# Kernel optimization log

Measured on AMD Instinct MI355X. Metric: run time of the kernel, lower is better.

The kernel has to match this reference:

```python
import jax, jax.numpy as jnp
import numpy as np

EPS = 1e-5
GROUPS = 32


def conv2d(x, w, b):
    # x: [N,C,H,W], w: [O,I,3,3] (or 1x1), stride 1, padding 'same' for 3x3
    kh = w.shape[2]
    pad = (kh - 1) // 2
    y = jax.lax.conv_general_dilated(x, w, (1, 1), ((pad, pad), (pad, pad)),
                                     dimension_numbers=('NCHW', 'OIHW', 'NCHW'))
    return y + b[None, :, None, None]


def group_norm(x, g, b):
    N, C, H, W = x.shape
    xr = x.reshape(N, GROUPS, C // GROUPS, H, W)
    mu = xr.mean(axis=(2, 3, 4), keepdims=True)
    var = xr.var(axis=(2, 3, 4), keepdims=True)
    xr = (xr - mu) / jnp.sqrt(var + EPS)
    return xr.reshape(N, C, H, W) * g[None, :, None, None] + b[None, :, None, None]


def batch_norm(x, g, b):
    # training-mode BatchNorm2d: batch statistics over (N,H,W)
    mu = x.mean(axis=(0, 2, 3), keepdims=True)
    var = x.var(axis=(0, 2, 3), keepdims=True)
    return (x - mu) / jnp.sqrt(var + EPS) * g[None, :, None, None] + b[None, :, None, None]


def binary_activation(x):
    # STE: forward sign(x), backward through piecewise poly out3
    out_fwd = jnp.sign(x)
    m1 = (x < -1).astype(x.dtype)
    m2 = (x < 0).astype(x.dtype)
    m3 = (x < 1).astype(x.dtype)
    out1 = -1.0 * m1 + (x * x + 2.0 * x) * (1.0 - m1)
    out2 = out1 * m2 + (-x * x + 2.0 * x) * (1.0 - m2)
    out3 = out2 * m3 + 1.0 * (1.0 - m3)
    return jax.lax.stop_gradient(out_fwd - out3) + out3


def hard_binary_conv(x, w, b):
    # per-output-channel scaling * sign(w), STE through clipped weights
    scale = jax.lax.stop_gradient(jnp.mean(jnp.abs(w), axis=(1, 2, 3), keepdims=True))
    bw_ng = scale * jnp.sign(w)
    clipped = jnp.clip(w, -1.0, 1.0)
    bw = jax.lax.stop_gradient(bw_ng - clipped) + clipped
    return conv2d(x, bw, b)


def learnable_bias(x, emb, w, b):
    bias = jax.nn.silu(emb) @ w.T + b  # [B, C]
    return x + bias[:, :, None, None]


def _forward(c, x, emb,
             rb_gn1_g, rb_gn1_b, rb_conv1_w, rb_conv1_b, rb_emb_w, rb_emb_b,
             rb_gn2_g, rb_gn2_b, rb_conv2_w, rb_conv2_b,
             m1_w, m1_b, bconv_w, bconv_b, bn_g, bn_b,
             m2_w, m2_b, prelu_a, m3_w, m3_b):
    # ResBlock (skip = Identity since out_channels == channels)
    h = conv2d(jax.nn.silu(group_norm(c, rb_gn1_g, rb_gn1_b)), rb_conv1_w, rb_conv1_b)
    eo = jax.nn.silu(emb) @ rb_emb_w.T + rb_emb_b          # [B, 2*C]
    scale, shift = jnp.split(eo[:, :, None, None], 2, axis=1)
    h = group_norm(h, rb_gn2_g, rb_gn2_b) * (1.0 + scale) + shift
    h = conv2d(jax.nn.silu(h), rb_conv2_w, rb_conv2_b)
    c2 = c + h
    # concat + bias + STE binarize + binary conv + BN + channel-pool residual + PReLU
    xc = jnp.concatenate([x, c2], axis=1)                   # [B, 2C, H, W]
    out = learnable_bias(xc, emb, m1_w, m1_b)
    out = binary_activation(out)
    out = hard_binary_conv(out, bconv_w, bconv_b)
    out = batch_norm(out, bn_g, bn_b)
    N, C2, H, W = xc.shape
    out = out + xc.reshape(N, C2 // 2, 2, H, W).mean(axis=2)  # channel mean pooling
    out = learnable_bias(out, emb, m2_w, m2_b)
    out = jnp.where(out >= 0, out, prelu_a[None, :, None, None] * out)  # PReLU
    out = learnable_bias(out, emb, m3_w, m3_b)
    return out


def setup_inputs() -> dict:
    key = jax.random.key(0)
    ks = jax.random.split(key, 24)
    B, C, EMB, H, W = 8, 128, 512, 64, 64
    IN2 = 2 * C
    n = lambda k, s, sc=0.05: jax.random.normal(k, s, dtype=jnp.float32) * sc
    return {
        'c': jax.random.normal(ks[0], (B, C, H, W), dtype=jnp.float32),
        'x': jax.random.normal(ks[1], (B, C, H, W), dtype=jnp.float32),
        'emb': jax.random.normal(ks[2], (B, EMB), dtype=jnp.float32),
        'rb_gn1_g': jnp.ones((C,), jnp.float32), 'rb_gn1_b': jnp.zeros((C,), jnp.float32),
        'rb_conv1_w': n(ks[3], (C, C, 3, 3)), 'rb_conv1_b': n(ks[4], (C,)),
        'rb_emb_w': n(ks[5], (2 * C, EMB)), 'rb_emb_b': n(ks[6], (2 * C,)),
        'rb_gn2_g': jnp.ones((C,), jnp.float32), 'rb_gn2_b': jnp.zeros((C,), jnp.float32),
        'rb_conv2_w': n(ks[7], (C, C, 3, 3)), 'rb_conv2_b': n(ks[8], (C,)),
        'm1_w': n(ks[9], (IN2, EMB)), 'm1_b': n(ks[10], (IN2,)),
        'bconv_w': jax.random.uniform(ks[11], (C, IN2, 3, 3), dtype=jnp.float32) * 0.001,
        'bconv_b': n(ks[12], (C,)),
        'bn_g': jnp.ones((C,), jnp.float32), 'bn_b': jnp.zeros((C,), jnp.float32),
        'm2_w': n(ks[13], (C, EMB)), 'm2_b': n(ks[14], (C,)),
        'prelu_a': jnp.full((C,), 0.25, jnp.float32),
        'm3_w': n(ks[15], (C, EMB)), 'm3_b': n(ks[16], (C,)),
    }


def reference(c, x, emb,
              rb_gn1_g, rb_gn1_b, rb_conv1_w, rb_conv1_b, rb_emb_w, rb_emb_b,
              rb_gn2_g, rb_gn2_b, rb_conv2_w, rb_conv2_b,
              m1_w, m1_b, bconv_w, bconv_b, bn_g, bn_b,
              m2_w, m2_b, prelu_a, m3_w, m3_b):
    return _forward(c, x, emb,
                    rb_gn1_g, rb_gn1_b, rb_conv1_w, rb_conv1_b, rb_emb_w, rb_emb_b,
                    rb_gn2_g, rb_gn2_b, rb_conv2_w, rb_conv2_b,
                    m1_w, m1_b, bconv_w, bconv_b, bn_g, bn_b,
                    m2_w, m2_b, prelu_a, m3_w, m3_b)
```

## Files before the change

### kernel.cpp

```cpp
#include <hip/hip_runtime.h>
#include <stdint.h>


#define B_   8
#define C_   128
#define C2_  256
#define HW_  4096
#define EMB_ 512
#define EPS_ 1e-5f

typedef int   v16i __attribute__((ext_vector_type(16)));
typedef float v16f __attribute__((ext_vector_type(16)));
typedef short v8s  __attribute__((ext_vector_type(8)));
typedef int   v4i  __attribute__((ext_vector_type(4)));

#define COLB 272
#define LDSZ (3 * 66 * COLB)

__device__ __forceinline__ float silu(float v) {
    return v * __builtin_amdgcn_rcpf(1.f + __expf(-v));
}
__device__ __forceinline__ unsigned short f2bf(float f) {
    unsigned int x = __float_as_uint(f);
    return (unsigned short)((x + 0x7FFFu + ((x >> 16) & 1u)) >> 16);
}
__device__ __forceinline__ int8_t sgn8(float v) {
    return (v > 0.f) ? (int8_t)1 : ((v < 0.f) ? (int8_t)(-1) : (int8_t)0);
}

__global__ __launch_bounds__(256) void k_prep(
    const float* __restrict__ w, int8_t* __restrict__ sgn,
    float* __restrict__ alpha, float* __restrict__ bnS, float* __restrict__ bnQ,
    float* __restrict__ gnS, float* __restrict__ gnQ,
    const float* __restrict__ w1, const float* __restrict__ w2,
    unsigned short* __restrict__ Wc1, unsigned short* __restrict__ Wc2,
    const float* __restrict__ emb,
    const float* __restrict__ ew, const float* __restrict__ ebb,
    const float* __restrict__ m1w, const float* __restrict__ m1b,
    const float* __restrict__ m2w, const float* __restrict__ m2b,
    const float* __restrict__ m3w, const float* __restrict__ m3b,
    float* __restrict__ eo, float* __restrict__ b1,
    float* __restrict__ b2, float* __restrict__ b3,
    const float* __restrict__ gin, const float* __restrict__ g1w,
    const float* __restrict__ g1b, unsigned short* __restrict__ act1) {
    __shared__ float red[256];
    const int blk = blockIdx.x, tid = threadIdx.x;
    if (blk < 128) {
        const int o = blk;
        if (o == 0 && tid < 128) { bnS[tid] = 0.f; bnQ[tid] = 0.f; }
        if (o == 1) { gnS[tid] = 0.f; }
        if (o == 2) { gnQ[tid] = 0.f; }
        const float* wr = w + (size_t)o * (C2_ * 9);
        float s = 0.f;
        for (int i = tid; i < C2_ * 9; i += 256) s += fabsf(wr[i]);
        red[tid] = s;
        __syncthreads();
        for (int st = 128; st > 0; st >>= 1) {
            if (tid < st) red[tid] += red[tid + st];
            __syncthreads();
        }
        if (tid == 0) alpha[o] = red[0] / (float)(C2_ * 9);
        for (int kk = 0; kk < 9; ++kk) {
            float v = wr[tid * 9 + kk];
            sgn[((size_t)(kk * 16 + (tid >> 4)) * C_ + o) * 16 + (tid & 15)] = sgn8(v);
        }
    } else if (blk < 704) {
        int i = (blk - 128) * 256 + tid;
        int co = i / (C_ * 9);
        int rem = i - co * (C_ * 9);
        int ci = rem / 9, kk = rem - ci * 9;
        size_t d = ((size_t)(kk * 16 + (ci >> 3)) * C_ + co) * 8 + (ci & 7);
        Wc1[d] = f2bf(w1[i]);
        Wc2[d] = f2bf(w2[i]);
    } else if (blk < 896) {
        const int o = (blk - 704) * 4 + (tid >> 6);
        const int l = tid & 63;
        const float* wv;
        float bias;
        float* dst;
        int dstride;
        if (o < 256)      { wv = ew  + (size_t)o * EMB_;              bias = ebb[o];    dst = eo + o;  dstride = 256; }
        else if (o < 512) { int r = o - 256; wv = m1w + (size_t)r * EMB_; bias = m1b[r]; dst = b1 + r; dstride = 256; }
        else if (o < 640) { int r = o - 512; wv = m2w + (size_t)r * EMB_; bias = m2b[r]; dst = b2 + r; dstride = 128; }
        else              { int r = o - 640; wv = m3w + (size_t)r * EMB_; bias = m3b[r]; dst = b3 + r; dstride = 128; }
        const float4 wa = *(const float4*)(wv + 8 * l);
        const float4 wb = *(const float4*)(wv + 8 * l + 4);
#pragma unroll
        for (int b = 0; b < B_; ++b) {
            const float* s = emb + b * EMB_ + 8 * l;
            float4 sa = *(const float4*)(s);
            float4 sb = *(const float4*)(s + 4);
            float p = wa.x * silu(sa.x) + wa.y * silu(sa.y) + wa.z * silu(sa.z) + wa.w * silu(sa.w) +
                      wb.x * silu(sb.x) + wb.y * silu(sb.y) + wb.z * silu(sb.z) + wb.w * silu(sb.w);
#pragma unroll
            for (int off = 32; off > 0; off >>= 1) p += __shfl_down(p, off, 64);
            if (l == 0) dst[b * dstride] = bias + p;
        }
    } else {
        const int bb = blk - 896;
        const int n = bb >> 5, grp = bb & 31;
        const size_t base = ((size_t)(n * C_ + grp * 4)) << 12;
        float sum = 0.f, sq = 0.f;
        const float4* in4 = (const float4*)(gin + base);
        for (int i = tid; i < 4096; i += 256) {
            float4 v = in4[i];
            sum += v.x + v.y + v.z + v.w;
            sq += v.x * v.x + v.y * v.y + v.z * v.z + v.w * v.w;
        }
#pragma unroll
        for (int off = 32; off > 0; off >>= 1) {
            sum += __shfl_xor(sum, off, 64);
            sq  += __shfl_xor(sq, off, 64);
        }
        if ((tid & 63) == 0) { red[tid >> 6] = sum; red[8 + (tid >> 6)] = sq; }
        __syncthreads();
        sum = red[0] + red[1] + red[2] + red[3];
        sq  = red[8] + red[9] + red[10] + red[11];
        const float mu = sum * (1.f / 16384.f);
        const float rstd = rsqrtf(sq * (1.f / 16384.f) - mu * mu + EPS_);
        float gg[4], bb4[4];
#pragma unroll
        for (int j = 0; j < 4; ++j) { gg[j] = g1w[grp * 4 + j]; bb4[j] = g1b[grp * 4 + j]; }
        for (int hw = tid; hw < HW_; hw += 256) {
            union { unsigned short u[4]; uint2 v; } pk;
#pragma unroll
            for (int j = 0; j < 4; ++j) {
                float v = gin[base + ((size_t)j << 12) + hw];
                pk.u[j] = f2bf(silu((v - mu) * rstd * gg[j] + bb4[j]));
            }
            *(uint2*)(act1 + ((size_t)(n * HW_ + hw)) * C_ + grp * 4) = pk.v;
        }
    }
}

__device__ __forceinline__ void stage_rows(char* lds, const char* rs0,
                                           const char* rs1, const char* rs2) {
    const int tid = threadIdx.x;
    const char* rs[3] = {rs0, rs1, rs2};
    if (tid < 96) {
        int r = tid / 32, q = tid & 31;
        int c = (q >> 4) ? 65 : 0, o = q & 15;
        *(float4*)(lds + (r * 66 + c) * COLB + o * 16) = make_float4(0.f, 0.f, 0.f, 0.f);
    }
#pragma unroll
    for (int u = 0; u < 12; ++u) {
        int idx = u * 256 + tid;
        int r = idx >> 10, rem = idx & 1023;
        int x = rem >> 4, o = rem & 15;
        char* dst = lds + (r * 66 + x + 1) * COLB + o * 16;
        if (rs[r]) *(float4*)dst = *(const float4*)(rs[r] + x * 256 + o * 16);
        else       *(float4*)dst = make_float4(0.f, 0.f, 0.f, 0.f);
    }
}

__global__ __launch_bounds__(256) void k_conv1(const unsigned short* __restrict__ act,
                                               const unsigned short* __restrict__ Wc,
                                               const float* __restrict__ bias,
                                               float* __restrict__ out,
                                               float* __restrict__ gnS,
                                               float* __restrict__ gnQ) {
    __shared__ __align__(16) char lds[LDSZ];
    const int y = blockIdx.x;
    const int n = blockIdx.y;
    const char* base = (const char*)(act + ((size_t)n * 64) * 64 * C_);
    stage_rows(lds,
               (y > 0)  ? base + (size_t)(y - 1) * 16384 : nullptr,
               base + (size_t)y * 16384,
               (y < 63) ? base + (size_t)(y + 1) * 16384 : nullptr);
    __syncthreads();

    const int w = threadIdx.x >> 6;
    const int l = threadIdx.x & 63;
    const int lm = l & 31;
    const int lh = l >> 5;

    v16f acc0, acc1;
#pragma unroll
    for (int i = 0; i < 16; ++i) { acc0[i] = 0.f; acc1[i] = 0.f; }

#pragma unroll
    for (int kk = 0; kk < 9; ++kk) {
        const int r = kk / 3, dx = kk % 3 - 1;
        const char* col0 = lds + (r * 66 + lm + 1 + dx) * COLB + 16 * lh;
        const char* col1 = col0 + 32 * COLB;
        const unsigned short* wbase = Wc + (size_t)(kk * 16 + lh) * C_ * 8 + (32 * w + lm) * 8;
#pragma unroll
        for (int cb = 0; cb < 8; ++cb) {
            v8s a = *(const v8s*)(wbase + (size_t)(2 * cb) * C_ * 8);
            v8s b0 = *(const v8s*)(col0 + 32 * cb);
            v8s b1 = *(const v8s*)(col1 + 32 * cb);
            acc0 = __builtin_amdgcn_mfma_f32_32x32x16_bf16(a, b0, acc0, 0, 0, 0);
            acc1 = __builtin_amdgcn_mfma_f32_32x32x16_bf16(a, b1, acc1, 0, 0, 0);
        }
    }
    float pr[16], qr[16];
#pragma unroll
    for (int r = 0; r < 16; ++r) {
        const int row = (r & 3) + 8 * (r >> 2) + 4 * lh;
        const int co = 32 * w + row;
        const float bv = bias[co];
        const size_t o = (((size_t)n * C_ + co) << 12) + (y << 6);
        float v0 = acc0[r] + bv, v1 = acc1[r] + bv;
        out[o + lm] = v0;
        out[o + 32 + lm] = v1;
        pr[r] = v0 + v1;
        qr[r] = v0 * v0 + v1 * v1;
    }
    __syncthreads();
    float* ldsS = (float*)lds;
    float* ldsQ = (float*)lds + 128;
#pragma unroll
    for (int r = 0; r < 16; ++r) {
        float p = pr[r], q = qr[r];
#pragma unroll
        for (int m = 16; m > 0; m >>= 1) {
            p += __shfl_xor(p, m, 64);
            q += __shfl_xor(q, m, 64);
        }
        if (lm == 0) {
            const int row = (r & 3) + 8 * (r >> 2) + 4 * lh;
            const int co = 32 * w + row;
            ldsS[co] = p;
            ldsQ[co] = q;
        }
    }
    __syncthreads();
    if (threadIdx.x < 32) {
        const int g = threadIdx.x;
        float p = ldsS[4 * g] + ldsS[4 * g + 1] + ldsS[4 * g + 2] + ldsS[4 * g + 3];
        float q = ldsQ[4 * g] + ldsQ[4 * g + 1] + ldsQ[4 * g + 2] + ldsQ[4 * g + 3];
        atomicAdd(&gnS[n * 32 + g], p);
        atomicAdd(&gnQ[n * 32 + g], q);
    }
}

__global__ __launch_bounds__(256) void k_conv2(const float* __restrict__ yin,
                                               const unsigned short* __restrict__ Wc,
                                               const float* __restrict__ bias,
                                               const float* __restrict__ res,
                                               const float* __restrict__ xin,
                                               const float* __restrict__ b1v,
                                               const float* __restrict__ eo,
                                               const float* __restrict__ g2,
                                               const float* __restrict__ bt2,
                                               const float* __restrict__ gnS,
                                               const float* __restrict__ gnQ,
                                               float* __restrict__ poolC2,
                                               int8_t* __restrict__ S) {
    __shared__ __align__(16) char lds[LDSZ];
    __shared__ float ldsA[128], ldsB[128];
    const int y = blockIdx.x;
    const int n = blockIdx.y;
    const int tid = threadIdx.x;

    if (tid < 128) {
        const int ch = tid, grp = tid >> 2;
        const float mu = gnS[n * 32 + grp] * (1.f / 16384.f);
        const float var = gnQ[n * 32 + grp] * (1.f / 16384.f) - mu * mu;
        const float rstd = rsqrtf(var + EPS_);
        const float gg = g2[ch] * rstd;
        const float sc = 1.f + eo[n * 256 + ch];
        ldsA[ch] = gg * sc;
        ldsB[ch] = (bt2[ch] - mu * gg) * sc + eo[n * 256 + 128 + ch];
    }
    if (tid < 96) {
        int r = tid / 32, q = tid & 31;
        int cpad = (q >> 4) ? 65 : 0, o = q & 15;
        *(float4*)(lds + (r * 66 + cpad) * COLB + o * 16) = make_float4(0.f, 0.f, 0.f, 0.f);
    }
    __syncthreads();

    const float* yb = yin + ((size_t)n * C_) * HW_ + (y << 6);
#pragma unroll 4
    for (int u = 0; u < 24; ++u) {
        int unit = u * 256 + tid;
        int r = unit >> 11, rem = unit & 2047;
        int ch = rem >> 4, seg = rem & 15;
        int yy = y - 1 + r;
        char* dst = lds + (r * 66 + 1 + seg) * COLB + ch * 2;
        if (yy >= 0 && yy < 64) {
            const float A = ldsA[ch], Bv = ldsB[ch];
            const float* src = yb + (size_t)ch * HW_ + (r - 1) * 64 + seg;
#pragma unroll
            for (int j = 0; j < 4; ++j)
                *(unsigned short*)(dst + (16 * j) * COLB) = f2bf(silu(src[16 * j] * A + Bv));
        } else {
#pragma unroll
            for (int j = 0; j < 4; ++j)
                *(unsigned short*)(dst + (16 * j) * COLB) = 0;
        }
    }
    __syncthreads();

    const int w = tid >> 6;
    const int l = tid & 63;
    const int lm = l & 31;
    const int lh = l >> 5;

    v16f acc0, acc1;
#pragma unroll
    for (int i = 0; i < 16; ++i) { acc0[i] = 0.f; acc1[i] = 0.f; }

#pragma unroll
    for (int kk = 0; kk < 9; ++kk) {
        const int r = kk / 3, dx = kk % 3 - 1;
        const char* col0 = lds + (r * 66 + lm + 1 + dx) * COLB + 16 * lh;
        const char* col1 = col0 + 32 * COLB;
        const unsigned short* wbase = Wc + (size_t)(kk * 16 + lh) * C_ * 8 + (32 * w + lm) * 8;
#pragma unroll
        for (int cb = 0; cb < 8; ++cb) {
            v8s a = *(const v8s*)(wbase + (size_t)(2 * cb) * C_ * 8);
            v8s b0 = *(const v8s*)(col0 + 32 * cb);
            v8s b1 = *(const v8s*)(col1 + 32 * cb);
            acc0 = __builtin_amdgcn_mfma_f32_32x32x16_bf16(a, b0, acc0, 0, 0, 0);
            acc1 = __builtin_amdgcn_mfma_f32_32x32x16_bf16(a, b1, acc1, 0, 0, 0);
        }
    }
    float c2v0[16], c2v1[16];
#pragma unroll
    for (int r = 0; r < 16; ++r) {
        const int row = (r & 3) + 8 * (r >> 2) + 4 * lh;
        const int co = 32 * w + row;
        const float bv = bias[co];
        const size_t o = (((size_t)n * C_ + co) << 12) + (y << 6);
        c2v0[r] = acc0[r] + bv + res[o + lm];
        c2v1[r] = acc1[r] + bv + res[o + 32 + lm];
    }
#pragma unroll
    for (int q = 0; q < 4; ++q) {
        const int pc = 16 * w + 4 * q + 2 * lh;
        const size_t po = (((size_t)n * 64 + pc) << 12) + (y << 6);
        poolC2[po + lm]             = 0.5f * (c2v0[4 * q] + c2v0[4 * q + 1]);
        poolC2[po + 32 + lm]        = 0.5f * (c2v1[4 * q] + c2v1[4 * q + 1]);
        poolC2[po + 4096 + lm]      = 0.5f * (c2v0[4 * q + 2] + c2v0[4 * q + 3]);
        poolC2[po + 4096 + 32 + lm] = 0.5f * (c2v1[4 * q + 2] + c2v1[4 * q + 3]);
    }

    __syncthreads();
#pragma unroll
    for (int q = 0; q < 4; ++q) {
        const int co0 = 32 * w + 8 * q + 4 * lh;
        const float b0 = b1v[n * 256 + 128 + co0];
        const float b1b = b1v[n * 256 + 128 + co0 + 1];
        const float b2b = b1v[n * 256 + 128 + co0 + 2];
        const float b3b = b1v[n * 256 + 128 + co0 + 3];
        union { int8_t b[4]; int u; } p0, p1;
        p0.b[0] = sgn8(c2v0[4 * q] + b0);  p1.b[0] = sgn8(c2v1[4 * q] + b0);
        p0.b[1] = sgn8(c2v0[4 * q + 1] + b1b); p1.b[1] = sgn8(c2v1[4 * q + 1] + b1b);
        p0.b[2] = sgn8(c2v0[4 * q + 2] + b2b); p1.b[2] = sgn8(c2v1[4 * q + 2] + b2b);
        p0.b[3] = sgn8(c2v0[4 * q + 3] + b3b); p1.b[3] = sgn8(c2v1[4 * q + 3] + b3b);
        *(int*)(lds + lm * COLB + 128 + co0) = p0.u;
        *(int*)(lds + (32 + lm) * COLB + 128 + co0) = p1.u;
    }
#pragma unroll
    for (int u = 0; u < 8; ++u) {
        int idx = u * 256 + tid;
        int ch = idx >> 4, seg = idx & 15;
        float4 v = *(const float4*)(xin + (((size_t)(n * C_ + ch)) << 12) + (y << 6) + 4 * seg);
        const float bv = b1v[n * 256 + ch];
        lds[(4 * seg) * COLB + ch]     = sgn8(v.x + bv);
        lds[(4 * seg + 1) * COLB + ch] = sgn8(v.y + bv);
        lds[(4 * seg + 2) * COLB + ch] = sgn8(v.z + bv);
        lds[(4 * seg + 3) * COLB + ch] = sgn8(v.w + bv);
    }
    __syncthreads();
    int8_t* Srow = S + ((size_t)(n * HW_) + (y << 6)) * C2_;
#pragma unroll
    for (int u = 0; u < 4; ++u) {
        int idx = u * 256 + tid;
        int px = idx >> 4, c16 = idx & 15;
        *(int4*)(Srow + (size_t)px * C2_ + 16 * c16) = *(const int4*)(lds + px * COLB + 16 * c16);
    }
}

__global__ __launch_bounds__(256) void k_bconv(const int8_t* __restrict__ S,
                                               const int8_t* __restrict__ Wk,
                                               const float* __restrict__ alpha,
                                               const float* __restrict__ bias,
                                               float* __restrict__ out,
                                               float* __restrict__ bnS,
                                               float* __restrict__ bnQ) {
    __shared__ __align__(16) char lds[LDSZ];
    const int y = blockIdx.x;
    const int n = blockIdx.y;
    const char* base = (const char*)(S + ((size_t)n * 64) * 64 * C2_);
    stage_rows(lds,
               (y > 0)  ? base + (size_t)(y - 1) * 16384 : nullptr,
               base + (size_t)y * 16384,
               (y < 63) ? base + (size_t)(y + 1) * 16384 : nullptr);
    __syncthreads();

    const int w = threadIdx.x >> 6;
    const int l = threadIdx.x & 63;
    const int lm = l & 31;
    const int lh = l >> 5;

    v16i acc0, acc1;
#pragma unroll
    for (int i = 0; i < 16; ++i) { acc0[i] = 0; acc1[i] = 0; }

#pragma unroll
    for (int kk = 0; kk < 9; ++kk) {
        const int r = kk / 3, dx = kk % 3 - 1;
        const char* col0 = lds + (r * 66 + lm + 1 + dx) * COLB + 16 * lh;
        const char* col1 = col0 + 32 * COLB;
        const int8_t* wbase = Wk + (size_t)(kk * 16 + lh) * C_ * 16 + (32 * w + lm) * 16;
#pragma unroll
        for (int s = 0; s < 8; ++s) {
            v4i a = *(const v4i*)(wbase + (size_t)(2 * s) * C_ * 16);
            v4i b0 = *(const v4i*)(col0 + 32 * s);
            v4i b1 = *(const v4i*)(col1 + 32 * s);
            acc0 = __builtin_amdgcn_mfma_i32_32x32x32_i8(a, b0, acc0, 0, 0, 0);
            acc1 = __builtin_amdgcn_mfma_i32_32x32x32_i8(a, b1, acc1, 0, 0, 0);
        }
    }

    float pr[16], qr[16];
#pragma unroll
    for (int r = 0; r < 16; ++r) {
        const int row = (r & 3) + 8 * (r >> 2) + 4 * lh;
        const int co = 32 * w + row;
        const float av = alpha[co], bv = bias[co];
        const size_t o = (((size_t)n * C_ + co) << 12) + (y << 6);
        float v0 = av * (float)acc0[r] + bv;
        float v1 = av * (float)acc1[r] + bv;
        out[o + lm]      = v0;
        out[o + 32 + lm] = v1;
        pr[r] = v0 + v1;
        qr[r] = v0 * v0 + v1 * v1;
    }
    __syncthreads();
    float* ldsS = (float*)lds;
    float* ldsQ = (float*)lds + 128;
#pragma unroll
    for (int r = 0; r < 16; ++r) {
        float p = pr[r], q = qr[r];
#pragma unroll
        for (int m = 16; m > 0; m >>= 1) {
            p += __shfl_xor(p, m, 64);
            q += __shfl_xor(q, m, 64);
        }
        if (lm == 0) {
            const int row = (r & 3) + 8 * (r >> 2) + 4 * lh;
            const int co = 32 * w + row;
            ldsS[co] = p;
            ldsQ[co] = q;
        }
    }
    __syncthreads();
    if (threadIdx.x < 128) {
        atomicAdd(&bnS[threadIdx.x], ldsS[threadIdx.x]);
        atomicAdd(&bnQ[threadIdx.x], ldsQ[threadIdx.x]);
    }
}

__global__ __launch_bounds__(256) void k_final(const float* __restrict__ y3,
                                               const float* __restrict__ x,
                                               const float* __restrict__ poolC2,
                                               const float* __restrict__ bnS,
                                               const float* __restrict__ bnQ,
                                               const float* __restrict__ bng,
                                               const float* __restrict__ bnb,
                                               const float* __restrict__ b2v,
                                               const float* __restrict__ pa,
                                               const float* __restrict__ b3v,
                                               float* __restrict__ out) {
    const int idx4 = blockIdx.x * 256 + threadIdx.x;
    const int hw = (idx4 & 1023) * 4;
    const int cb = idx4 >> 10;
    const int co = cb & 127;
    const int n = cb >> 7;
    const float mu = bnS[co] * (1.f / 32768.f);
    const float var = bnQ[co] * (1.f / 32768.f) - mu * mu;
    const float rstd = rsqrtf(var + EPS_);
    const float gm = rstd * bng[co];
    const float bt = bnb[co] - mu * gm;
    const size_t obase = (((size_t)(n * C_ + co)) << 12) + hw;
    float4 v = *(const float4*)(y3 + obase);
    v.x = v.x * gm + bt; v.y = v.y * gm + bt; v.z = v.z * gm + bt; v.w = v.w * gm + bt;

    float4 pv;
    if (co < 64) {
        const int ch0 = 2 * co;
        float4 pA = *(const float4*)(x + (((size_t)(n * C_ + ch0)) << 12) + hw);
        float4 pB = *(const float4*)(x + (((size_t)(n * C_ + ch0 + 1)) << 12) + hw);
        pv.x = 0.5f * (pA.x + pB.x); pv.y = 0.5f * (pA.y + pB.y);
        pv.z = 0.5f * (pA.z + pB.z); pv.w = 0.5f * (pA.w + pB.w);
    } else {
        pv = *(const float4*)(poolC2 + (((size_t)(n * 64 + co - 64)) << 12) + hw);
    }
    const float bias2 = b2v[n * 128 + co];
    const float aP = pa[co];
    const float bias3 = b3v[n * 128 + co];
    float4 r;
    float t;
    t = v.x + pv.x + bias2; t = (t >= 0.f) ? t : aP * t; r.x = t + bias3;
    t = v.y + pv.y + bias2; t = (t >= 0.f) ? t : aP * t; r.y = t + bias3;
    t = v.z + pv.z + bias2; t = (t >= 0.f) ? t : aP * t; r.z = t + bias3;
    t = v.w + pv.w + bias2; t = (t >= 0.f) ? t : aP * t; r.w = t + bias3;
    *(float4*)(out + obase) = r;
}

extern "C" void kernel_launch(void* const* d_in, const int* in_sizes, int n_in,
                              void* d_out, int out_size, void* d_ws, size_t ws_size,
                              hipStream_t stream) {
    const float* c       = (const float*)d_in[0];
    const float* x       = (const float*)d_in[1];
    const float* emb     = (const float*)d_in[2];
    const float* gn1_g   = (const float*)d_in[3];
    const float* gn1_b   = (const float*)d_in[4];
    const float* conv1_w = (const float*)d_in[5];
    const float* conv1_b = (const float*)d_in[6];
    const float* emb_w   = (const float*)d_in[7];
    const float* emb_b   = (const float*)d_in[8];
    const float* gn2_g   = (const float*)d_in[9];
    const float* gn2_b   = (const float*)d_in[10];
    const float* conv2_w = (const float*)d_in[11];
    const float* conv2_b = (const float*)d_in[12];
    const float* m1_w    = (const float*)d_in[13];
    const float* m1_b    = (const float*)d_in[14];
    const float* bconv_w = (const float*)d_in[15];
    const float* bconv_b = (const float*)d_in[16];
    const float* bn_g    = (const float*)d_in[17];
    const float* bn_b    = (const float*)d_in[18];
    const float* m2_w    = (const float*)d_in[19];
    const float* m2_b    = (const float*)d_in[20];
    const float* prelu_a = (const float*)d_in[21];
    const float* m3_w    = (const float*)d_in[22];
    const float* m3_b    = (const float*)d_in[23];
    float* out = (float*)d_out;

    float* ws = (float*)d_ws;
    const size_t NCHW = (size_t)B_ * C_ * HW_;
    float*  poolC2 = ws;
    float*  y_buf = ws + NCHW;
    unsigned short* actA = (unsigned short*)(ws + 2 * NCHW);
    int8_t* S     = (int8_t*)(ws + 2 * NCHW);
    int8_t* sgn   = (int8_t*)(ws + 2 * NCHW + NCHW / 2);
    unsigned short* Wc1 = (unsigned short*)(ws + 2 * NCHW + NCHW / 2 + 73728);
    unsigned short* Wc2 = Wc1 + C_ * C_ * 9;
    float*  alpha = ws + 2 * NCHW + NCHW / 2 + 73728 + 2 * 73728;
    float*  eo    = alpha + 128;
    float*  b1v   = eo + B_ * 256;
    float*  b2v   = b1v + B_ * 256;
    float*  b3v   = b2v + B_ * 128;
    float*  bnS   = b3v + B_ * 128;
    float*  bnQ   = bnS + 128;
    float*  gnS   = bnQ + 128;
    float*  gnQ   = gnS + 256;

    k_prep<<<1152, 256, 0, stream>>>(bconv_w, sgn, alpha, bnS, bnQ, gnS, gnQ,
                                     conv1_w, conv2_w, Wc1, Wc2,
                                     emb, emb_w, emb_b, m1_w, m1_b, m2_w, m2_b,
                                     m3_w, m3_b, eo, b1v, b2v, b3v,
                                     c, gn1_g, gn1_b, actA);
    k_conv1<<<dim3(64, B_), 256, 0, stream>>>(actA, Wc1, conv1_b, y_buf, gnS, gnQ);
    k_conv2<<<dim3(64, B_), 256, 0, stream>>>(y_buf, Wc2, conv2_b, c, x, b1v, eo,
                                              gn2_g, gn2_b, gnS, gnQ, poolC2, S);
    k_bconv<<<dim3(64, B_), 256, 0, stream>>>(S, sgn, alpha, bconv_b, y_buf, bnS, bnQ);
    k_final<<<NCHW / 1024, 256, 0, stream>>>(y_buf, x, poolC2, bnS, bnQ, bn_g, bn_b,
                                             b2v, prelu_a, b3v, out);
}
```

Baseline: 237.4 us.

## Store conv1 output pixel-major via LDS transpose and vectorize conv2/prep staging

```diff
diff --git a/kernel.cpp b/kernel.cpp
--- a/kernel.cpp
+++ b/kernel.cpp
@@ -16,6 +16,7 @@
 
 #define COLB 272
 #define LDSZ (3 * 66 * COLB)
+#define TSTRIDE 132
 
 __device__ __forceinline__ float silu(float v) {
     return v * __builtin_amdgcn_rcpf(1.f + __expf(-v));
@@ -26,6 +27,30 @@
 }
 __device__ __forceinline__ int8_t sgn8(float v) {
     return (v > 0.f) ? (int8_t)1 : ((v < 0.f) ? (int8_t)(-1) : (int8_t)0);
+}
+
+__device__ __forceinline__ void stage_one(char* lds, int r, const char* src) {
+    const int tid = threadIdx.x;
+#pragma unroll
+    for (int it = 0; it < 4; ++it) {
+        int idx = it * 256 + tid;
+        int x = idx >> 4, o = idx & 15;
+        char* dst = lds + (r * 66 + x + 1) * COLB + o * 16;
+        if (src) *(float4*)dst = *(const float4*)(src + x * 256 + o * 16);
+        else     *(float4*)dst = make_float4(0.f, 0.f, 0.f, 0.f);
+    }
+}
+__device__ __forceinline__ void stage3(char* lds, const char* r0,
+                                       const char* r1, const char* r2) {
+    const int tid = threadIdx.x;
+    if (tid < 96) {
+        int r = tid / 32, q = tid & 31;
+        int c = (q >> 4) ? 65 : 0, o = q & 15;
+        *(float4*)(lds + (r * 66 + c) * COLB + o * 16) = make_float4(0.f, 0.f, 0.f, 0.f);
+    }
+    stage_one(lds, 0, r0);
+    stage_one(lds, 1, r1);
+    stage_one(lds, 2, r2);
 }
 
 __global__ __launch_bounds__(256) void k_prep(
@@ -121,52 +146,39 @@
         float gg[4], bb4[4];
 #pragma unroll
         for (int j = 0; j < 4; ++j) { gg[j] = g1w[grp * 4 + j]; bb4[j] = g1b[grp * 4 + j]; }
-        for (int hw = tid; hw < HW_; hw += 256) {
-            union { unsigned short u[4]; uint2 v; } pk;
-#pragma unroll
-            for (int j = 0; j < 4; ++j) {
-                float v = gin[base + ((size_t)j << 12) + hw];
-                pk.u[j] = f2bf(silu((v - mu) * rstd * gg[j] + bb4[j]));
+        union F4 { float4 v; float f[4]; };
+        for (int i = tid; i < 1024; i += 256) {
+            const int hw = 4 * i;
+            F4 vj[4];
+#pragma unroll
+            for (int j = 0; j < 4; ++j)
+                vj[j].v = *(const float4*)(gin + base + ((size_t)j << 12) + hw);
+#pragma unroll
+            for (int e = 0; e < 4; ++e) {
+                union { unsigned short u[4]; uint2 v; } pk;
+#pragma unroll
+                for (int j = 0; j < 4; ++j)
+                    pk.u[j] = f2bf(silu((vj[j].f[e] - mu) * rstd * gg[j] + bb4[j]));
+                *(uint2*)(act1 + ((size_t)(n * HW_ + hw + e)) * C_ + grp * 4) = pk.v;
             }
-            *(uint2*)(act1 + ((size_t)(n * HW_ + hw)) * C_ + grp * 4) = pk.v;
-        }
-    }
-}
-
-__device__ __forceinline__ void stage_rows(char* lds, const char* rs0,
-                                           const char* rs1, const char* rs2) {
-    const int tid = threadIdx.x;
-    const char* rs[3] = {rs0, rs1, rs2};
-    if (tid < 96) {
-        int r = tid / 32, q = tid & 31;
-        int c = (q >> 4) ? 65 : 0, o = q & 15;
-        *(float4*)(lds + (r * 66 + c) * COLB + o * 16) = make_float4(0.f, 0.f, 0.f, 0.f);
-    }
-#pragma unroll
-    for (int u = 0; u < 12; ++u) {
-        int idx = u * 256 + tid;
-        int r = idx >> 10, rem = idx & 1023;
-        int x = rem >> 4, o = rem & 15;
-        char* dst = lds + (r * 66 + x + 1) * COLB + o * 16;
-        if (rs[r]) *(float4*)dst = *(const float4*)(rs[r] + x * 256 + o * 16);
-        else       *(float4*)dst = make_float4(0.f, 0.f, 0.f, 0.f);
+        }
     }
 }
 
 __global__ __launch_bounds__(256) void k_conv1(const unsigned short* __restrict__ act,
                                                const unsigned short* __restrict__ Wc,
                                                const float* __restrict__ bias,
-                                               float* __restrict__ out,
+                                               float* __restrict__ outN,
                                                float* __restrict__ gnS,
                                                float* __restrict__ gnQ) {
     __shared__ __align__(16) char lds[LDSZ];
     const int y = blockIdx.x;
     const int n = blockIdx.y;
     const char* base = (const char*)(act + ((size_t)n * 64) * 64 * C_);
-    stage_rows(lds,
-               (y > 0)  ? base + (size_t)(y - 1) * 16384 : nullptr,
-               base + (size_t)y * 16384,
-               (y < 63) ? base + (size_t)(y + 1) * 16384 : nullptr);
+    stage3(lds,
+           (y > 0)  ? base + (size_t)(y - 1) * 16384 : nullptr,
+           base + (size_t)y * 16384,
+           (y < 63) ? base + (size_t)(y + 1) * 16384 : nullptr);
     __syncthreads();
 
     const int w = threadIdx.x >> 6;
@@ -193,36 +205,35 @@
             acc1 = __builtin_amdgcn_mfma_f32_32x32x16_bf16(a, b1, acc1, 0, 0, 0);
         }
     }
-    float pr[16], qr[16];
+    float sv0[16], sv1[16], pr[16], qr[16];
 #pragma unroll
     for (int r = 0; r < 16; ++r) {
         const int row = (r & 3) + 8 * (r >> 2) + 4 * lh;
         const int co = 32 * w + row;
         const float bv = bias[co];
-        const size_t o = (((size_t)n * C_ + co) << 12) + (y << 6);
         float v0 = acc0[r] + bv, v1 = acc1[r] + bv;
-        out[o + lm] = v0;
-        out[o + 32 + lm] = v1;
+        sv0[r] = v0;
+        sv1[r] = v1;
         pr[r] = v0 + v1;
         qr[r] = v0 * v0 + v1 * v1;
     }
     __syncthreads();
-    float* ldsS = (float*)lds;
-    float* ldsQ = (float*)lds + 128;
+    float* ldsT = (float*)lds;
+    float* ldsS = (float*)(lds + 64 * TSTRIDE * 4);
+    float* ldsQ = ldsS + 128;
 #pragma unroll
     for (int r = 0; r < 16; ++r) {
+        const int row = (r & 3) + 8 * (r >> 2) + 4 * lh;
+        const int co = 32 * w + row;
+        ldsT[lm * TSTRIDE + co] = sv0[r];
+        ldsT[(32 + lm) * TSTRIDE + co] = sv1[r];
         float p = pr[r], q = qr[r];
 #pragma unroll
         for (int m = 16; m > 0; m >>= 1) {
             p += __shfl_xor(p, m, 64);
             q += __shfl_xor(q, m, 64);
         }
-        if (lm == 0) {
-            const int row = (r & 3) + 8 * (r >> 2) + 4 * lh;
-            const int co = 32 * w + row;
-            ldsS[co] = p;
-            ldsQ[co] = q;
-        }
+        if (lm == 0) { ldsS[co] = p; ldsQ[co] = q; }
     }
     __syncthreads();
     if (threadIdx.x < 32) {
@@ -231,6 +242,14 @@
         float q = ldsQ[4 * g] + ldsQ[4 * g + 1] + ldsQ[4 * g + 2] + ldsQ[4 * g + 3];
         atomicAdd(&gnS[n * 32 + g], p);
         atomicAdd(&gnQ[n * 32 + g], q);
+    }
+    const int q4 = threadIdx.x & 31;
+    float* orow = outN + (((size_t)(n * HW_) + (y << 6)) << 7);
+#pragma unroll
+    for (int it = 0; it < 8; ++it) {
+        const int px = it * 8 + (threadIdx.x >> 5);
+        *(float4*)(orow + ((size_t)px << 7) + 4 * q4) =
+            *(const float4*)(ldsT + px * TSTRIDE + 4 * q4);
     }
 }
 
@@ -270,24 +289,29 @@
     }
     __syncthreads();
 
-    const float* yb = yin + ((size_t)n * C_) * HW_ + (y << 6);
-#pragma unroll 4
-    for (int u = 0; u < 24; ++u) {
-        int unit = u * 256 + tid;
-        int r = unit >> 11, rem = unit & 2047;
-        int ch = rem >> 4, seg = rem & 15;
-        int yy = y - 1 + r;
-        char* dst = lds + (r * 66 + 1 + seg) * COLB + ch * 2;
-        if (yy >= 0 && yy < 64) {
-            const float A = ldsA[ch], Bv = ldsB[ch];
-            const float* src = yb + (size_t)ch * HW_ + (r - 1) * 64 + seg;
-#pragma unroll
-            for (int j = 0; j < 4; ++j)
-                *(unsigned short*)(dst + (16 * j) * COLB) = f2bf(silu(src[16 * j] * A + Bv));
-        } else {
-#pragma unroll
-            for (int j = 0; j < 4; ++j)
-                *(unsigned short*)(dst + (16 * j) * COLB) = 0;
+    const int qc = tid & 31;
+    float A0 = ldsA[4 * qc], A1 = ldsA[4 * qc + 1], A2 = ldsA[4 * qc + 2], A3 = ldsA[4 * qc + 3];
+    float B0 = ldsB[4 * qc], B1 = ldsB[4 * qc + 1], B2 = ldsB[4 * qc + 2], B3 = ldsB[4 * qc + 3];
+#pragma unroll
+    for (int r = 0; r < 3; ++r) {
+        const int yy = y - 1 + r;
+        const float* ysrc = yin + (((size_t)(n * HW_) + yy * 64) << 7);
+        const bool ok = (yy >= 0 && yy < 64);
+#pragma unroll
+        for (int it = 0; it < 8; ++it) {
+            const int px = it * 8 + (tid >> 5);
+            char* dst = lds + (r * 66 + px + 1) * COLB + qc * 8;
+            if (ok) {
+                float4 v = *(const float4*)(ysrc + ((size_t)px << 7) + 4 * qc);
+                union { unsigned short u[4]; uint2 q; } pk;
+                pk.u[0] = f2bf(silu(v.x * A0 + B0));
+                pk.u[1] = f2bf(silu(v.y * A1 + B1));
+                pk.u[2] = f2bf(silu(v.z * A2 + B2));
+                pk.u[3] = f2bf(silu(v.w * A3 + B3));
+                *(uint2*)dst = pk.q;
+            } else {
+                *(uint2*)dst = make_uint2(0u, 0u);
+            }
         }
     }
     __syncthreads();
@@ -345,7 +369,7 @@
         const float b2b = b1v[n * 256 + 128 + co0 + 2];
         const float b3b = b1v[n * 256 + 128 + co0 + 3];
         union { int8_t b[4]; int u; } p0, p1;
-        p0.b[0] = sgn8(c2v0[4 * q] + b0);  p1.b[0] = sgn8(c2v1[4 * q] + b0);
+        p0.b[0] = sgn8(c2v0[4 * q] + b0);      p1.b[0] = sgn8(c2v1[4 * q] + b0);
         p0.b[1] = sgn8(c2v0[4 * q + 1] + b1b); p1.b[1] = sgn8(c2v1[4 * q + 1] + b1b);
         p0.b[2] = sgn8(c2v0[4 * q + 2] + b2b); p1.b[2] = sgn8(c2v1[4 * q + 2] + b2b);
         p0.b[3] = sgn8(c2v0[4 * q + 3] + b3b); p1.b[3] = sgn8(c2v1[4 * q + 3] + b3b);
@@ -384,10 +408,10 @@
     const int y = blockIdx.x;
     const int n = blockIdx.y;
     const char* base = (const char*)(S + ((size_t)n * 64) * 64 * C2_);
-    stage_rows(lds,
-               (y > 0)  ? base + (size_t)(y - 1) * 16384 : nullptr,
-               base + (size_t)y * 16384,
-               (y < 63) ? base + (size_t)(y + 1) * 16384 : nullptr);
+    stage3(lds,
+           (y > 0)  ? base + (size_t)(y - 1) * 16384 : nullptr,
+           base + (size_t)y * 16384,
+           (y < 63) ? base + (size_t)(y + 1) * 16384 : nullptr);
     __syncthreads();
 
     const int w = threadIdx.x >> 6;
```

Measured after the change: 242.7 us. +2.2%, slower.
